# Optimization experiments

Hardware: AMD Instinct MI355X
Metric: run time of the kernel (lower is better)

The kernel has to match this reference:

```python
import jax, jax.numpy as jnp
import numpy as np

T, N = 20, 192
D_EMB, D_H, D_REL = 32, 64, 32
D_TMP = D_REL + 2 * D_H  # 160 = rel_emb + h_self + h_neighbor


def setup_inputs() -> dict:
    key = jax.random.key(0)
    ks = jax.random.split(key, 16)
    g = lambda i, shape, s: jax.random.normal(ks[i], shape, jnp.float32) * s
    inp = {
        "nodes_abs": g(0, (T, N, 2), 1.0),
        "nodes_norm": g(1, (T, N, 2), 1.0),
        "shift_value": g(2, (T, N, 2), 1.0),
        # parameters (inputLayer, LSTMCell, 2 GCNs, outputLayer)
        "w_in": g(3, (D_EMB, 2), 0.2),
        "b_in": jnp.zeros((D_EMB,), jnp.float32),
        "w_ih": g(4, (4 * D_H, D_EMB), 0.1),
        "w_hh": g(5, (4 * D_H, D_H), 0.001),
        "b_ih": jnp.zeros((4 * D_H,), jnp.float32).at[D_H:2 * D_H].set(1.0),
        "b_hh": jnp.zeros((4 * D_H,), jnp.float32),
        "w_rel": g(6, (2, D_REL, 2), 0.1),
        "b_rel": jnp.zeros((2, D_REL), jnp.float32),
        "w_gate": g(7, (2, D_H, D_TMP), 0.1),
        "b_gate": jnp.zeros((2, D_H), jnp.float32),
        "w_ar": g(8, (2, D_TMP), 0.1),
        "b_ar": jnp.zeros((2,), jnp.float32),
        "w_nei": g(9, (2, D_H, D_H), 0.1),
        "w_out": g(10, (2, D_H), 0.1),
        "b_out": jnp.zeros((2,), jnp.float32),
        # int inputs
        "seq_list": jax.random.randint(ks[11], (T, N), 0, 2).astype(jnp.int32),
        "nei_list": jax.random.randint(ks[12], (T, N, N), 0, 2).astype(jnp.int32),
        "nei_num": jax.random.randint(ks[13], (T, N), 0, N).astype(jnp.int32),
    }
    return inp


def reference(nodes_abs, nodes_norm, shift_value, w_in, b_in, w_ih, w_hh, b_ih, b_hh,
              w_rel, b_rel, w_gate, b_gate, w_ar, b_ar, w_nei, w_out, b_out,
              seq_list, nei_list, nei_num):
    eps = 1e-6

    def gcn(p, corr, nei_f, h, c, o):
        # corr: (N,N,2) relative positions pos_i - pos_j; nei_f: (N,N) 0/1 mask
        r = jax.nn.relu(jnp.einsum('ijd,rd->ijr', corr, w_rel[p]) + b_rel[p])
        tmp = jnp.concatenate([r,
                               jnp.broadcast_to(h[:, None, :], (N, N, D_H)),
                               jnp.broadcast_to(h[None, :, :], (N, N, D_H))], axis=-1)
        gate = jax.nn.sigmoid(jnp.einsum('ijt,ht->ijh', tmp, w_gate[p]) + b_gate[p])
        score = jnp.einsum('ijt,t->ij', tmp, w_ar[p]) + b_ar[p]
        score = jnp.where(nei_f > 0, score, -1e9)
        pos = jax.nn.softmax(score, axis=1) * nei_f  # masked attention over neighbors j
        msg = jnp.einsum('ij,ijh,jh->ih', pos, gate, h)  # gated, attended aggregation
        c_new = c + msg @ w_nei[p].T
        h_new = o * jnp.tanh(c_new)
        v1 = jnp.sum(gate * nei_f[:, :, None]) / (jnp.sum(nei_f) * D_H + eps)
        v2 = jnp.sum(jnp.max(pos, axis=1)) / (jnp.sum(jnp.max(nei_f, axis=1)) + eps)
        v3 = jnp.sum(nei_f) / jnp.float32(N)
        return h_new, c_new, (v1, v2, v3)

    def step(carry, xs):
        h, c, v1s, v2s, v3s = carry
        abs_t, norm_t, seq_t, nei_t = xs
        m = seq_t > 0
        mf = m.astype(jnp.float32)
        nei_f = (nei_t > 0).astype(jnp.float32) * mf[:, None] * mf[None, :]
        corr = abs_t[:, None, :] - abs_t[None, :, :]  # corr_index[i,j] = pos_i - pos_j
        x = jax.nn.relu(norm_t @ w_in.T + b_in)  # dropout is identity in eval
        gates = x @ w_ih.T + b_ih + h @ w_hh.T + b_hh
        i_g, f_g, g_g, o_g = jnp.split(gates, 4, axis=-1)
        i_g = jax.nn.sigmoid(i_g); f_g = jax.nn.sigmoid(f_g); o_g = jax.nn.sigmoid(o_g)
        c1 = f_g * c + i_g * jnp.tanh(g_g)
        h1 = o_g * jnp.tanh(c1)
        h1, c1, look = gcn(0, corr, nei_f, h1, c1, o_g)
        h1, c1, _ = gcn(1, corr, nei_f, h1, c1, o_g)
        out_t = (h1 @ w_out.T + b_out) * mf[:, None]
        h = jnp.where(m[:, None], h1, h)  # only active nodes update state
        c = jnp.where(m[:, None], c1, c)
        return (h, c, v1s + look[0], v2s + look[1], v3s + look[2]), out_t

    h0 = jnp.zeros((N, D_H), jnp.float32)
    c0 = jnp.zeros((N, D_H), jnp.float32)
    z = jnp.float32(0.0)
    xs = (nodes_abs[:-1], nodes_norm[:-1], seq_list[:-1], nei_list[:-1])
    (h, c, v1, v2, v3), outs = jax.lax.scan(step, (h0, c0, z, z, z), xs)
    outputs = jnp.concatenate([outs, jnp.zeros((1, N, 2), jnp.float32)], axis=0)
    return outputs, h, c, (v1 / T, v2 / T, v3 / T)
```

## Files before the change

### kernel.cpp

```cpp
#include <hip/hip_runtime.h>
#include <hip/hip_bf16.h>

#define T_STEPS 20
#define NSTEP   19
#define NN      192
#define DH      64
#define DE      32

enum : int {
  O_H     = 0,
  O_C     = O_H    + NN*DH,
  O_UH0   = O_C    + NN*DH,
  O_UH1   = O_UH0  + 2*NN*DH,
  O_CW    = O_UH1  + 2*NN*DH,
  O_OG    = O_CW   + NN*DH,
  O_U1    = O_OG   + NN*DH,
  O_S1    = O_U1   + NN*DH,
  O_S20   = O_S1   + NN,
  O_S21   = O_S20  + NN,
  O_ACC   = O_S21  + NN,
  O_WIHT  = O_ACC  + NSTEP*4 + 4,
  O_WHHT  = O_WIHT + 8192,
  O_BIH   = O_WHHT + 16384,
  O_WIN   = O_BIH  + 256,
  O_BIN   = O_WIN  + 64,
  O_WRELF = O_BIN  + 32,
  O_BRELF = O_WRELF+ 128,
  O_WGR   = O_BRELF+ 64,
  O_WGH1T = O_WGR  + 4096,
  O_WGH2T = O_WGH1T+ 8192,
  O_BGATE = O_WGH2T+ 8192,
  O_WARR  = O_BGATE+ 128,
  O_WARH1 = O_WARR + 64,
  O_WARH2 = O_WARH1+ 128,
  O_BAR   = O_WARH2+ 128,
  O_WNEIT = O_BAR  + 4,
  O_WOUT  = O_WNEIT+ 8192,
  O_BOUT  = O_WOUT + 128,
  O_ISF   = O_BOUT + 2,
  O_TOTAL = O_ISF  + 1
};

typedef unsigned long long ull;

__device__ __forceinline__ float bf2f(__hip_bfloat16 v) { return __bfloat162float(v); }
__device__ __forceinline__ float sigm(float x) { return 1.0f / (1.0f + __expf(-x)); }
__device__ __forceinline__ float tanh_fast(float x) {
  float e = __expf(-2.0f * fabsf(x));
  float r = (1.0f - e) / (1.0f + e);
  return copysignf(r, x);
}

__device__ __forceinline__ float ldf(const void* p, int idx, int isf32) {
  if (isf32) return ((const float*)p)[idx];
  return bf2f(((const __hip_bfloat16*)p)[idx]);
}
__device__ __forceinline__ void stf(void* p, int idx, float v, int isf32) {
  if (isf32) ((float*)p)[idx] = v;
  else       ((__hip_bfloat16*)p)[idx] = __float2bfloat16(v);
}

__device__ __forceinline__ int resolve_isf(const float* F, int isf_arg) {
  return (isf_arg >= 0) ? isf_arg : (int)F[O_ISF];
}

__device__ __forceinline__ void lstm_prep_dev(
    float* __restrict__ F, const void* __restrict__ nnorm, int isf32,
    int t, int i, int tid, int wave, int lane, int load_hc,
    float* s_x, float* s_hc, float* s_cc, float* s_gates, float* s_h1)
{
  if (load_hc && wave == 0) { s_hc[lane] = F[O_H + i*DH + lane]; s_cc[lane] = F[O_C + i*DH + lane]; }
  if (wave == 1 && lane < DE) {
    float nx = ldf(nnorm, (t*NN + i)*2 + 0, isf32);
    float ny = ldf(nnorm, (t*NN + i)*2 + 1, isf32);
    s_x[lane] = fmaxf(nx*F[O_WIN + lane*2] + ny*F[O_WIN + lane*2 + 1] + F[O_BIN + lane], 0.f);
  }
  __syncthreads();
  {
    int G = tid;
    float acc = F[O_BIH + G];
    for (int e = 0; e < DE; e++) acc += F[O_WIHT + e*256 + G] * s_x[e];
    for (int k = 0; k < DH; k++) acc += F[O_WHHT + k*256 + G] * s_hc[k];
    s_gates[G] = acc;
  }
  __syncthreads();
  if (wave == 0) {
    float ig = sigm(s_gates[lane]);
    float fg = sigm(s_gates[64 + lane]);
    float gg = tanh_fast(s_gates[128 + lane]);
    float og = sigm(s_gates[192 + lane]);
    float c1 = fg * s_cc[lane] + ig * gg;
    float h1 = og * tanh_fast(c1);
    int idx = i*DH + lane;
    F[O_CW  + idx] = c1;
    F[O_UH0 + 2*idx + 1] = h1;
    F[O_OG  + idx] = og;
    s_h1[lane] = h1;
  }
  __syncthreads();
  {
    int idx = i*DH + lane;
    if (wave == 0) {
      float a = 0.f;
      const float* w = F + O_WGH1T + lane;
      for (int k = 0; k < DH; k++) a += w[k*DH] * s_h1[k];
      F[O_U1 + idx] = a;
    } else if (wave == 1) {
      float a = 0.f;
      const float* w = F + O_WGH2T + lane;
      for (int k = 0; k < DH; k++) a += w[k*DH] * s_h1[k];
      F[O_UH0 + 2*idx] = a;
    } else if (wave == 2) {
      float hp = s_h1[lane];
      float a1 = hp * F[O_WARH1 + lane];
      float a2 = hp * F[O_WARH2 + lane];
      for (int o = 32; o >= 1; o >>= 1) { a1 += __shfl_xor(a1, o, 64); a2 += __shfl_xor(a2, o, 64); }
      if (lane == 0) { F[O_S1 + i] = a1; F[O_S20 + i] = a2; }
    }
  }
}

__global__ __launch_bounds__(256) void k_init(float* __restrict__ F,
                       void* __restrict__ out,
                       const void* w_in,  const void* b_in,
                       const void* w_ih,  const void* w_hh,
                       const void* b_ih,  const void* b_hh,
                       const void* w_rel, const void* b_rel,
                       const void* w_gate,const void* b_gate,
                       const void* w_ar,  const void* b_ar,
                       const void* w_nei, const void* w_out,
                       const void* b_out, int isf_arg) {
  __shared__ int s_isf;
  const int wave = threadIdx.x >> 6, lane = threadIdx.x & 63;
  if (isf_arg >= 0) {
    if (threadIdx.x == 0) s_isf = isf_arg;
  } else if (wave == 0) {
    const unsigned short* u = (const unsigned short*)w_gate;
    int bad = 0;
    for (int x = lane; x < 1024; x += 64) {
      float v = __uint_as_float(((unsigned)u[x]) << 16);
      if (!(fabsf(v) <= 4.0f)) bad++;
    }
    for (int o = 32; o >= 1; o >>= 1) bad += __shfl_xor(bad, o, 64);
    if (lane == 0) s_isf = (bad > 64);
  }
  __syncthreads();
  const int isf32 = s_isf;
  if (blockIdx.x == 0 && threadIdx.x == 0) F[O_ISF] = (float)isf32;

  int tid = blockIdx.x * blockDim.x + threadIdx.x;
  int stride = gridDim.x * blockDim.x;
  for (int x = tid; x < O_WIHT; x += stride) F[x] = 0.f;
  for (int x = tid; x < NN*2;  x += stride) stf(out, (T_STEPS-1)*NN*2 + x, 0.f, isf32);
  for (int x = tid; x < 8192;  x += stride) { int e = x >> 8, G = x & 255; F[O_WIHT + x] = ldf(w_ih, G*32 + e, isf32); }
  for (int x = tid; x < 16384; x += stride) { int k = x >> 8, G = x & 255; F[O_WHHT + x] = ldf(w_hh, G*64 + k, isf32); }
  for (int x = tid; x < 256;   x += stride) F[O_BIH + x] = ldf(b_ih, x, isf32) + ldf(b_hh, x, isf32);
  for (int x = tid; x < 64;    x += stride) F[O_WIN + x] = ldf(w_in, x, isf32);
  for (int x = tid; x < 32;    x += stride) F[O_BIN + x] = ldf(b_in, x, isf32);
  for (int x = tid; x < 128;   x += stride) F[O_WRELF + x] = ldf(w_rel, x, isf32);
  for (int x = tid; x < 64;    x += stride) F[O_BRELF + x] = ldf(b_rel, x, isf32);
  for (int x = tid; x < 4096;  x += stride) { int p = x >> 11, h = (x >> 5) & 63, d = x & 31;
    F[O_WGR + x] = ldf(w_gate, p*10240 + h*160 + d, isf32); }
  for (int x = tid; x < 8192;  x += stride) { int p = x >> 12, k = (x >> 6) & 63, h = x & 63;
    F[O_WGH1T + x] = ldf(w_gate, p*10240 + h*160 + 32 + k, isf32); }
  for (int x = tid; x < 8192;  x += stride) { int p = x >> 12, k = (x >> 6) & 63, h = x & 63;
    F[O_WGH2T + x] = ldf(w_gate, p*10240 + h*160 + 96 + k, isf32); }
  for (int x = tid; x < 128;   x += stride) F[O_BGATE + x] = ldf(b_gate, x, isf32);
  for (int x = tid; x < 64;    x += stride) { int p = x >> 5, d = x & 31; F[O_WARR + x] = ldf(w_ar, p*160 + d, isf32); }
  for (int x = tid; x < 128;   x += stride) { int p = x >> 6, k = x & 63; F[O_WARH1 + x] = ldf(w_ar, p*160 + 32 + k, isf32); }
  for (int x = tid; x < 128;   x += stride) { int p = x >> 6, k = x & 63; F[O_WARH2 + x] = ldf(w_ar, p*160 + 96 + k, isf32); }
  for (int x = tid; x < 2;     x += stride) F[O_BAR + x] = ldf(b_ar, x, isf32);
  for (int x = tid; x < 8192;  x += stride) { int p = x >> 12, k = (x >> 6) & 63, h = x & 63;
    F[O_WNEIT + x] = ldf(w_nei, p*4096 + h*64 + k, isf32); }
  for (int x = tid; x < 128;   x += stride) F[O_WOUT + x] = ldf(w_out, x, isf32);
  for (int x = tid; x < 2;     x += stride) F[O_BOUT + x] = ldf(b_out, x, isf32);
}

__global__ __launch_bounds__(256) void k_lstm0(float* __restrict__ F,
                                               const void* __restrict__ nnorm,
                                               int isf_arg) {
  __shared__ float s_x[DE], s_hc[DH], s_cc[DH], s_gates[4*DH], s_h1[DH];
  const int tid = threadIdx.x, wave = tid >> 6, lane = tid & 63;
  const int isf32 = resolve_isf(F, isf_arg);
  lstm_prep_dev(F, nnorm, isf32, 0, blockIdx.x, tid, wave, lane, 1,
                s_x, s_hc, s_cc, s_gates, s_h1);
}

__global__ __launch_bounds__(256) void k_gcn(float* __restrict__ F,
                                             const void* __restrict__ nabs,
                                             const void* __restrict__ nnorm,
                                             const int* __restrict__ seq,
                                             const int* __restrict__ nei,
                                             void* __restrict__ out,
                                             int t, int p, int last,
                                             int isf_arg) {
  __shared__ float s_rt[NN*33];
  __shared__ float s_score[NN], s_pos[NN], s_neif[NN];
  __shared__ int   s_jlist[NN];
  __shared__ ull   s_cmask[3];
  __shared__ float s_red[4*DH], s_v1[4], s_msg[DH], s_hprep[DH];
  __shared__ float s_x[DE], s_hc[DH], s_cc[DH], s_gates[4*DH], s_h1[DH];

  const int tid = threadIdx.x, wave = tid >> 6, lane = tid & 63;
  const int i = blockIdx.x;
  const int isf32 = resolve_isf(F, isf_arg);
  const int m_i = seq[t*NN + i] > 0;
  const int UHr = p ? O_UH1 : O_UH0;
  const int S2r = p ? O_S21 : O_S20;

  const int j = wave*64 + lane;
  ull mymask = 0; int nf = 0;
  if (wave < 3) {
    nf = m_i && (seq[t*NN + j] > 0) && (nei[(t*NN + i)*NN + j] > 0);
    s_neif[j] = nf ? 1.f : 0.f;
    mymask = __ballot(nf != 0);
    if (lane == 0) s_cmask[wave] = mymask;
  }
  __syncthreads();
  const int c0 = __popcll(s_cmask[0]), c1 = __popcll(s_cmask[1]), c2 = __popcll(s_cmask[2]);
  const int nv = c0 + c1 + c2;
  if (wave < 3 && nf) {
    int base = (wave == 0) ? 0 : (wave == 1 ? c0 : c0 + c1);
    ull lt = (1ull << lane) - 1ull;
    s_jlist[base + __popcll(mymask & lt)] = j;
  }
  __syncthreads();

  const float2* UH2 = (const float2*)(F + UHr);
  int jc[8]; float2 uc[8];
#pragma unroll
  for (int q = 0; q < 8; q++) {
    int kk = wave + q*4;
    jc[q] = (kk < nv) ? s_jlist[kk] : -1;
    uc[q] = make_float2(0.f, 0.f);
    if (jc[q] >= 0) uc[q] = UH2[jc[q]*DH + lane];
  }
  if (wave < 3) {
    float sc = 0.f;
    if (nf) {
      float cx = ldf(nabs, (t*NN + i)*2 + 0, isf32) - ldf(nabs, (t*NN + j)*2 + 0, isf32);
      float cy = ldf(nabs, (t*NN + i)*2 + 1, isf32) - ldf(nabs, (t*NN + j)*2 + 1, isf32);
      const float* wr = F + O_WRELF + p*64;
      const float* br = F + O_BRELF + p*32;
      const float* wa = F + O_WARR  + p*32;
      float dot = 0.f;
#pragma unroll
      for (int d = 0; d < 32; d++) {
        float rv = fmaxf(cx*wr[2*d] + cy*wr[2*d+1] + br[d], 0.f);
        s_rt[j*33 + d] = rv;
        dot += rv * wa[d];
      }
      sc = dot + F[O_S1 + i] + F[S2r + j] + F[O_BAR + p];
    }
    s_score[j] = sc;
  }
  __syncthreads();

  if (wave == 0) {
    float n0 = s_neif[lane], n1 = s_neif[64+lane], n2 = s_neif[128+lane];
    float sc0 = s_score[lane], sc1 = s_score[64+lane], sc2 = s_score[128+lane];
    const float NEG = -3.0e38f;
    float mx = fmaxf(fmaxf(n0 > 0.f ? sc0 : NEG, n1 > 0.f ? sc1 : NEG),
                     n2 > 0.f ? sc2 : NEG);
    for (int o = 32; o >= 1; o >>= 1) mx = fmaxf(mx, __shfl_xor(mx, o, 64));
    float e0 = (n0 > 0.f) ? __expf(sc0 - mx) : 0.f;
    float e1 = (n1 > 0.f) ? __expf(sc1 - mx) : 0.f;
    float e2 = (n2 > 0.f) ? __expf(sc2 - mx) : 0.f;
    float s = e0 + e1 + e2;
    for (int o = 32; o >= 1; o >>= 1) s += __shfl_xor(s, o, 64);
    float inv = (s > 0.f) ? 1.0f / s : 0.f;
    float p0 = e0*inv, p1 = e1*inv, p2 = e2*inv;
    s_pos[lane] = p0; s_pos[64+lane] = p1; s_pos[128+lane] = p2;
    if (p == 0 && m_i) {
      float cnt = n0 + n1 + n2;
      float pm  = fmaxf(fmaxf(p0, p1), p2);
      for (int o = 32; o >= 1; o >>= 1) {
        cnt += __shfl_xor(cnt, o, 64);
        pm   = fmaxf(pm, __shfl_xor(pm, o, 64));
      }
      if (lane == 0 && cnt > 0.f) {
        atomicAdd(&F[O_ACC + t*4 + 1], cnt);
        atomicAdd(&F[O_ACC + t*4 + 2], pm);
        atomicAdd(&F[O_ACC + t*4 + 3], 1.f);
      }
    }
  }
  __syncthreads();

  {
    float msg = 0.f, v1 = 0.f;
    if (m_i && nv > 0) {
      float wreg[32];
      const float* wgp = F + O_WGR + p*2048 + lane*32;
#pragma unroll
      for (int d = 0; d < 32; d++) wreg[d] = wgp[d];
      float basev = F[O_U1 + i*DH + lane] + F[O_BGATE + p*DH + lane];
      for (int k = wave; k < nv; k += 32) {
        int jn[8]; float2 un[8];
#pragma unroll
        for (int q = 0; q < 8; q++) {
          int kk = k + 32 + q*4;
          jn[q] = (kk < nv) ? s_jlist[kk] : -1;
          un[q] = make_float2(0.f, 0.f);
          if (jn[q] >= 0) un[q] = UH2[jn[q]*DH + lane];
        }
#pragma unroll
        for (int q = 0; q < 8; q++) {
          if (jc[q] >= 0) {
            float acc = basev + uc[q].x;
            const float* rr = &s_rt[jc[q]*33];
#pragma unroll
            for (int d = 0; d < 32; d++) acc += rr[d] * wreg[d];
            float g = sigm(acc);
            v1 += g;
            msg += s_pos[jc[q]] * g * uc[q].y;
          }
        }
#pragma unroll
        for (int q = 0; q < 8; q++) { jc[q] = jn[q]; uc[q] = un[q]; }
      }
    }
    s_red[wave*DH + lane] = msg;
    for (int o = 32; o >= 1; o >>= 1) v1 += __shfl_xor(v1, o, 64);
    if (lane == 0) s_v1[wave] = v1;
  }
  __syncthreads();

  if (wave == 0) {
    s_msg[lane] = s_red[lane] + s_red[64+lane] + s_red[128+lane] + s_red[192+lane];
    if (p == 0 && m_i && lane == 0) {
      float v1t = s_v1[0] + s_v1[1] + s_v1[2] + s_v1[3];
      atomicAdd(&F[O_ACC + t*4 + 0], v1t);
    }
  }
  __syncthreads();

  if (wave == 0) {
    int idx = i*DH + lane;
    float hcom, ccom = 0.f;
    if (m_i) {
      float cn = F[O_CW + idx];
      const float* wn = F + O_WNEIT + p*4096 + lane;
      for (int k = 0; k < DH; k++) cn += s_msg[k] * wn[k*DH];
      hcom = F[O_OG + idx] * tanh_fast(cn);
      F[O_CW + idx] = cn;
      ccom = cn;
      if (p == 1) { F[O_H + idx] = hcom; F[O_C + idx] = ccom; }
    } else {
      hcom = F[UHr + 2*idx + 1];
    }
    if (p == 0) F[O_UH1 + 2*idx + 1] = hcom;
    s_hprep[lane] = hcom;
    if (p == 1) {
      s_hc[lane] = m_i ? hcom : F[O_H + idx];
      s_cc[lane] = m_i ? ccom : F[O_C + idx];
    }
  }
  __syncthreads();

  if (p == 0) {
    int idx = i*DH + lane;
    if (wave == 0) {
      float a = 0.f;
      const float* w = F + O_WGH1T + 4096 + lane;
      for (int k = 0; k < DH; k++) a += w[k*DH] * s_hprep[k];
      F[O_U1 + idx] = a;
    } else if (wave == 1) {
      float a = 0.f;
      const float* w = F + O_WGH2T + 4096 + lane;
      for (int k = 0; k < DH; k++) a += w[k*DH] * s_hprep[k];
      F[O_UH1 + 2*idx] = a;
    } else if (wave == 2) {
      float hp = s_hprep[lane];
      float a1 = hp * F[O_WARH1 + DH + lane];
      float a2 = hp * F[O_WARH2 + DH + lane];
      for (int o = 32; o >= 1; o >>= 1) { a1 += __shfl_xor(a1, o, 64); a2 += __shfl_xor(a2, o, 64); }
      if (lane == 0) { F[O_S1 + i] = a1; F[O_S21 + i] = a2; }
    }
  } else {
    if (wave == 0 && lane < 2) {
      float a = 0.f;
      if (m_i) {
        a = F[O_BOUT + lane];
        const float* wo = F + O_WOUT + lane*DH;
        for (int h = 0; h < DH; h++) a += s_hprep[h] * wo[h];
      }
      stf(out, (t*NN + i)*2 + lane, a, isf32);
    }
    if (!last) {
      lstm_prep_dev(F, nnorm, isf32, t + 1, i, tid, wave, lane, 0,
                    s_x, s_hc, s_cc, s_gates, s_h1);
    } else {
      if (wave == 0) stf(out, T_STEPS*NN*2 + i*DH + lane,         s_hc[lane], isf32);
      if (wave == 1) stf(out, T_STEPS*NN*2 + NN*DH + i*DH + lane, s_cc[lane], isf32);
      if (i == 0 && tid == 0) {
        float v1 = 0.f, v2 = 0.f, v3 = 0.f;
        for (int tt = 0; tt < NSTEP; tt++) {
          float sg = F[O_ACC + tt*4 + 0], sn = F[O_ACC + tt*4 + 1];
          float sp = F[O_ACC + tt*4 + 2], sm = F[O_ACC + tt*4 + 3];
          v1 += sg / (sn * 64.f + 1e-6f);
          v2 += sp / (sm + 1e-6f);
          v3 += sn / 192.f;
        }
        int base = T_STEPS*NN*2 + 2*NN*DH;
        stf(out, base + 0, v1 / 20.f, isf32);
        stf(out, base + 1, v2 / 20.f, isf32);
        stf(out, base + 2, v3 / 20.f, isf32);
      }
    }
  }
}

extern "C" void kernel_launch(void* const* d_in, const int* in_sizes, int n_in,
                              void* d_out, int out_size, void* d_ws, size_t ws_size,
                              hipStream_t stream) {
  const void* nabs  = d_in[0];
  const void* nnorm = d_in[1];
  const int* seq = (const int*)d_in[18];
  const int* nei = (const int*)d_in[19];
  float* F = (float*)d_ws;

  int isf = -1;
  if (n_in > 11 && in_sizes) {
    if      (in_sizes[11] == 81920) isf = 1;
    else if (in_sizes[11] == 40960) isf = 0;
  }

  k_init<<<NN, 256, 0, stream>>>(F, d_out,
      d_in[3], d_in[4], d_in[5], d_in[6], d_in[7], d_in[8], d_in[9], d_in[10],
      d_in[11], d_in[12], d_in[13], d_in[14], d_in[15], d_in[16], d_in[17], isf);
  k_lstm0<<<NN, 256, 0, stream>>>(F, nnorm, isf);
  for (int t = 0; t < NSTEP; t++) {
    k_gcn<<<NN, 256, 0, stream>>>(F, nabs, nnorm, seq, nei, d_out, t, 0, 0, isf);
    k_gcn<<<NN, 256, 0, stream>>>(F, nabs, nnorm, seq, nei, d_out, t, 1, t == NSTEP - 1, isf);
  }
}
```

Before: 697.8 us.

## Fuse all timesteps into one persistent kernel with a software grid barrier

Replaces the 39 per-step kernel launches with a single persistent kernel of 192 blocks that synchronises through an atomic grid barrier using coherent (sc0 sc1) loads and stores. Per-node state (c, og, u1, s1) is kept in shared memory, LSTM weights are held in registers, and the gate and other small weights are cached in LDS, removing repeated global reloads. The rel-gate weight layout is transposed to suit the new LDS access pattern. The risk is deadlock if not all 192 blocks are co-resident, and the spin barrier itself adds latency on every step.

```diff
diff --git a/kernel.cpp b/kernel.cpp
--- a/kernel.cpp
+++ b/kernel.cpp
@@ -19,7 +19,8 @@
   O_S20   = O_S1   + NN,
   O_S21   = O_S20  + NN,
   O_ACC   = O_S21  + NN,
-  O_WIHT  = O_ACC  + NSTEP*4 + 4,
+  O_GBAR  = O_ACC  + NSTEP*4,
+  O_WIHT  = O_GBAR + 4,
   O_WHHT  = O_WIHT + 8192,
   O_BIH   = O_WHHT + 16384,
   O_WIN   = O_BIH  + 256,
@@ -60,64 +61,52 @@
   else       ((__hip_bfloat16*)p)[idx] = __float2bfloat16(v);
 }
 
-__device__ __forceinline__ int resolve_isf(const float* F, int isf_arg) {
-  return (isf_arg >= 0) ? isf_arg : (int)F[O_ISF];
-}
-
-__device__ __forceinline__ void lstm_prep_dev(
-    float* __restrict__ F, const void* __restrict__ nnorm, int isf32,
-    int t, int i, int tid, int wave, int lane, int load_hc,
-    float* s_x, float* s_hc, float* s_cc, float* s_gates, float* s_h1)
-{
-  if (load_hc && wave == 0) { s_hc[lane] = F[O_H + i*DH + lane]; s_cc[lane] = F[O_C + i*DH + lane]; }
-  if (wave == 1 && lane < DE) {
-    float nx = ldf(nnorm, (t*NN + i)*2 + 0, isf32);
-    float ny = ldf(nnorm, (t*NN + i)*2 + 1, isf32);
-    s_x[lane] = fmaxf(nx*F[O_WIN + lane*2] + ny*F[O_WIN + lane*2 + 1] + F[O_BIN + lane], 0.f);
-  }
-  __syncthreads();
-  {
-    int G = tid;
-    float acc = F[O_BIH + G];
-    for (int e = 0; e < DE; e++) acc += F[O_WIHT + e*256 + G] * s_x[e];
-    for (int k = 0; k < DH; k++) acc += F[O_WHHT + k*256 + G] * s_hc[k];
-    s_gates[G] = acc;
-  }
-  __syncthreads();
-  if (wave == 0) {
-    float ig = sigm(s_gates[lane]);
-    float fg = sigm(s_gates[64 + lane]);
-    float gg = tanh_fast(s_gates[128 + lane]);
-    float og = sigm(s_gates[192 + lane]);
-    float c1 = fg * s_cc[lane] + ig * gg;
-    float h1 = og * tanh_fast(c1);
-    int idx = i*DH + lane;
-    F[O_CW  + idx] = c1;
-    F[O_UH0 + 2*idx + 1] = h1;
-    F[O_OG  + idx] = og;
-    s_h1[lane] = h1;
-  }
-  __syncthreads();
-  {
-    int idx = i*DH + lane;
-    if (wave == 0) {
-      float a = 0.f;
-      const float* w = F + O_WGH1T + lane;
-      for (int k = 0; k < DH; k++) a += w[k*DH] * s_h1[k];
-      F[O_U1 + idx] = a;
-    } else if (wave == 1) {
-      float a = 0.f;
-      const float* w = F + O_WGH2T + lane;
-      for (int k = 0; k < DH; k++) a += w[k*DH] * s_h1[k];
-      F[O_UH0 + 2*idx] = a;
-    } else if (wave == 2) {
-      float hp = s_h1[lane];
-      float a1 = hp * F[O_WARH1 + lane];
-      float a2 = hp * F[O_WARH2 + lane];
-      for (int o = 32; o >= 1; o >>= 1) { a1 += __shfl_xor(a1, o, 64); a2 += __shfl_xor(a2, o, 64); }
-      if (lane == 0) { F[O_S1 + i] = a1; F[O_S20 + i] = a2; }
+__device__ __forceinline__ ull ld_coh_u64_async(const void* p) {
+  ull v;
+  asm volatile("global_load_dwordx2 %0, %1, off sc0 sc1" : "=v"(v) : "v"(p));
+  return v;
+}
+__device__ __forceinline__ float ld_coh_f32_async(const void* p) {
+  float v;
+  asm volatile("global_load_dword %0, %1, off sc0 sc1" : "=v"(v) : "v"(p));
+  return v;
+}
+__device__ __forceinline__ float ld_coh_f32(const void* p) {
+  float v;
+  asm volatile("global_load_dword %0, %1, off sc0 sc1\n\ts_waitcnt vmcnt(0)"
+               : "=v"(v) : "v"(p) : "memory");
+  return v;
+}
+__device__ __forceinline__ unsigned ld_coh_u32(const void* p) {
+  unsigned v;
+  asm volatile("global_load_dword %0, %1, off sc0 sc1\n\ts_waitcnt vmcnt(0)"
+               : "=v"(v) : "v"(p) : "memory");
+  return v;
+}
+__device__ __forceinline__ void st_coh_f32(void* p, float v) {
+  asm volatile("global_store_dword %0, %1, off sc0 sc1" :: "v"(p), "v"(v) : "memory");
+}
+__device__ __forceinline__ void st_coh_u32(void* p, unsigned v) {
+  asm volatile("global_store_dword %0, %1, off sc0 sc1" :: "v"(p), "v"(v) : "memory");
+}
+__device__ __forceinline__ void vm_wait0() {
+  asm volatile("s_waitcnt vmcnt(0)" ::: "memory");
+  __builtin_amdgcn_sched_barrier(0);
+}
+
+__device__ __forceinline__ void gridbar(float* F, unsigned ep) {
+  asm volatile("s_waitcnt vmcnt(0)" ::: "memory");
+  __syncthreads();
+  if (threadIdx.x == 0) {
+    unsigned* bar = (unsigned*)(F + O_GBAR);
+    unsigned v = atomicAdd(bar, 1u) + 1u;
+    if (v == (ep + 1u) * (unsigned)NN) {
+      st_coh_u32(bar + 1, ep + 1u);
+    } else {
+      while (ld_coh_u32(bar + 1) < ep + 1u) __builtin_amdgcn_s_sleep(2);
     }
   }
+  __syncthreads();
 }
 
 __global__ __launch_bounds__(256) void k_init(float* __restrict__ F,
@@ -159,7 +148,7 @@
   for (int x = tid; x < 32;    x += stride) F[O_BIN + x] = ldf(b_in, x, isf32);
   for (int x = tid; x < 128;   x += stride) F[O_WRELF + x] = ldf(w_rel, x, isf32);
   for (int x = tid; x < 64;    x += stride) F[O_BRELF + x] = ldf(b_rel, x, isf32);
-  for (int x = tid; x < 4096;  x += stride) { int p = x >> 11, h = (x >> 5) & 63, d = x & 31;
+  for (int x = tid; x < 4096;  x += stride) { int p = x >> 11, d = (x >> 6) & 31, h = x & 63;
     F[O_WGR + x] = ldf(w_gate, p*10240 + h*160 + d, isf32); }
   for (int x = tid; x < 8192;  x += stride) { int p = x >> 12, k = (x >> 6) & 63, h = x & 63;
     F[O_WGH1T + x] = ldf(w_gate, p*10240 + h*160 + 32 + k, isf32); }
@@ -176,236 +165,302 @@
   for (int x = tid; x < 2;     x += stride) F[O_BOUT + x] = ldf(b_out, x, isf32);
 }
 
-__global__ __launch_bounds__(256) void k_lstm0(float* __restrict__ F,
-                                               const void* __restrict__ nnorm,
-                                               int isf_arg) {
-  __shared__ float s_x[DE], s_hc[DH], s_cc[DH], s_gates[4*DH], s_h1[DH];
-  const int tid = threadIdx.x, wave = tid >> 6, lane = tid & 63;
-  const int isf32 = resolve_isf(F, isf_arg);
-  lstm_prep_dev(F, nnorm, isf32, 0, blockIdx.x, tid, wave, lane, 1,
-                s_x, s_hc, s_cc, s_gates, s_h1);
-}
-
-__global__ __launch_bounds__(256) void k_gcn(float* __restrict__ F,
-                                             const void* __restrict__ nabs,
-                                             const void* __restrict__ nnorm,
-                                             const int* __restrict__ seq,
-                                             const int* __restrict__ nei,
-                                             void* __restrict__ out,
-                                             int t, int p, int last,
-                                             int isf_arg) {
+__device__ __forceinline__ void lstm_prep(
+    float* __restrict__ F, const void* __restrict__ nnorm, int isf32,
+    int t, int i, int tid, int wave, int lane,
+    const float* wih_r, const float* whh_r, float bih_r,
+    const float* s_win, const float* s_cB,
+    float* s_x, float* s_hc, float* s_cc, float* s_gates, float* s_h1,
+    float* s_cw, float* s_og, float* s_u1, float* s_s1)
+{
+  if (wave == 1 && lane < DE) {
+    float nx = ldf(nnorm, (t*NN + i)*2 + 0, isf32);
+    float ny = ldf(nnorm, (t*NN + i)*2 + 1, isf32);
+    s_x[lane] = fmaxf(nx*s_win[lane*2] + ny*s_win[lane*2 + 1] + s_win[64 + lane], 0.f);
+  }
+  __syncthreads();
+  {
+    float acc = bih_r;
+#pragma unroll
+    for (int e = 0; e < DE; e++) acc += wih_r[e] * s_x[e];
+#pragma unroll
+    for (int k = 0; k < DH; k++) acc += whh_r[k] * s_hc[k];
+    s_gates[tid] = acc;
+  }
+  __syncthreads();
+  if (wave == 0) {
+    float ig = sigm(s_gates[lane]);
+    float fg = sigm(s_gates[64 + lane]);
+    float gg = tanh_fast(s_gates[128 + lane]);
+    float og = sigm(s_gates[192 + lane]);
+    float c1 = fg * s_cc[lane] + ig * gg;
+    float h1 = og * tanh_fast(c1);
+    s_cw[lane] = c1;
+    s_og[lane] = og;
+    s_h1[lane] = h1;
+    st_coh_f32(F + O_UH0 + 2*(i*DH + lane) + 1, h1);
+  }
+  __syncthreads();
+  if (wave == 0) {
+    float a = 0.f;
+    const float* w = F + O_WGH1T + lane;
+    for (int k = 0; k < DH; k++) a += w[k*DH] * s_h1[k];
+    s_u1[lane] = a;
+  } else if (wave == 1) {
+    float a = 0.f;
+    const float* w = F + O_WGH2T + lane;
+    for (int k = 0; k < DH; k++) a += w[k*DH] * s_h1[k];
+    st_coh_f32(F + O_UH0 + 2*(i*DH + lane), a);
+  } else if (wave == 2) {
+    float hp = s_h1[lane];
+    float a1 = hp * s_cB[192 + lane];
+    float a2 = hp * s_cB[320 + lane];
+    for (int o = 32; o >= 1; o >>= 1) { a1 += __shfl_xor(a1, o, 64); a2 += __shfl_xor(a2, o, 64); }
+    if (lane == 0) { *s_s1 = a1; st_coh_f32(F + O_S20 + i, a2); }
+  }
+}
+
+__global__ __launch_bounds__(256, 1) void k_main(float* __restrict__ F,
+    const void* __restrict__ nabs, const void* __restrict__ nnorm,
+    const int* __restrict__ seq, const int* __restrict__ nei,
+    void* __restrict__ out, int isf_arg)
+{
   __shared__ float s_rt[NN*33];
   __shared__ float s_score[NN], s_pos[NN], s_neif[NN];
   __shared__ int   s_jlist[NN];
   __shared__ ull   s_cmask[3];
   __shared__ float s_red[4*DH], s_v1[4], s_msg[DH], s_hprep[DH];
   __shared__ float s_x[DE], s_hc[DH], s_cc[DH], s_gates[4*DH], s_h1[DH];
+  __shared__ float s_cw[DH], s_og[DH], s_u1[DH], s_s1;
+  __shared__ float s_wgt[4096];
+  __shared__ float s_cA[192], s_cB[452], s_cC[130], s_win[96];
+  __shared__ float s_fin[NSTEP*4];
 
   const int tid = threadIdx.x, wave = tid >> 6, lane = tid & 63;
   const int i = blockIdx.x;
-  const int isf32 = resolve_isf(F, isf_arg);
-  const int m_i = seq[t*NN + i] > 0;
-  const int UHr = p ? O_UH1 : O_UH0;
-  const int S2r = p ? O_S21 : O_S20;
-
-  const int j = wave*64 + lane;
-  ull mymask = 0; int nf = 0;
-  if (wave < 3) {
-    nf = m_i && (seq[t*NN + j] > 0) && (nei[(t*NN + i)*NN + j] > 0);
-    s_neif[j] = nf ? 1.f : 0.f;
-    mymask = __ballot(nf != 0);
-    if (lane == 0) s_cmask[wave] = mymask;
-  }
-  __syncthreads();
-  const int c0 = __popcll(s_cmask[0]), c1 = __popcll(s_cmask[1]), c2 = __popcll(s_cmask[2]);
-  const int nv = c0 + c1 + c2;
-  if (wave < 3 && nf) {
-    int base = (wave == 0) ? 0 : (wave == 1 ? c0 : c0 + c1);
-    ull lt = (1ull << lane) - 1ull;
-    s_jlist[base + __popcll(mymask & lt)] = j;
-  }
-  __syncthreads();
-
-  const float2* UH2 = (const float2*)(F + UHr);
-  int jc[8]; float2 uc[8];
-#pragma unroll
-  for (int q = 0; q < 8; q++) {
-    int kk = wave + q*4;
-    jc[q] = (kk < nv) ? s_jlist[kk] : -1;
-    uc[q] = make_float2(0.f, 0.f);
-    if (jc[q] >= 0) uc[q] = UH2[jc[q]*DH + lane];
-  }
-  if (wave < 3) {
-    float sc = 0.f;
-    if (nf) {
-      float cx = ldf(nabs, (t*NN + i)*2 + 0, isf32) - ldf(nabs, (t*NN + j)*2 + 0, isf32);
-      float cy = ldf(nabs, (t*NN + i)*2 + 1, isf32) - ldf(nabs, (t*NN + j)*2 + 1, isf32);
-      const float* wr = F + O_WRELF + p*64;
-      const float* br = F + O_BRELF + p*32;
-      const float* wa = F + O_WARR  + p*32;
-      float dot = 0.f;
-#pragma unroll
-      for (int d = 0; d < 32; d++) {
-        float rv = fmaxf(cx*wr[2*d] + cy*wr[2*d+1] + br[d], 0.f);
-        s_rt[j*33 + d] = rv;
-        dot += rv * wa[d];
-      }
-      sc = dot + F[O_S1 + i] + F[S2r + j] + F[O_BAR + p];
+  const int isf32 = (isf_arg >= 0) ? isf_arg : (int)F[O_ISF];
+
+  float wih_r[DE], whh_r[DH];
+  const float bih_r = F[O_BIH + tid];
+#pragma unroll
+  for (int e = 0; e < DE; e++) wih_r[e] = F[O_WIHT + e*256 + tid];
+#pragma unroll
+  for (int k = 0; k < DH; k++) whh_r[k] = F[O_WHHT + k*256 + tid];
+
+  for (int x = tid; x < 4096; x += 256) s_wgt[x] = F[O_WGR + x];
+  for (int x = tid; x < 192; x += 256) s_cA[x] = F[O_WRELF + x];
+  for (int x = tid; x < 452; x += 256) s_cB[x] = F[O_BGATE + x];
+  for (int x = tid; x < 130; x += 256) s_cC[x] = F[O_WOUT + x];
+  for (int x = tid; x < 96;  x += 256) s_win[x] = F[O_WIN + x];
+  if (wave == 0) { s_hc[lane] = 0.f; s_cc[lane] = 0.f; }
+  __syncthreads();
+
+  lstm_prep(F, nnorm, isf32, 0, i, tid, wave, lane,
+            wih_r, whh_r, bih_r, s_win, s_cB,
+            s_x, s_hc, s_cc, s_gates, s_h1, s_cw, s_og, s_u1, &s_s1);
+
+  unsigned ep = 0;
+  for (int t = 0; t < NSTEP; ++t) {
+    const int m_i = seq[t*NN + i] > 0;
+    const int j = wave*64 + lane;
+
+    ull mymask = 0; int nf = 0;
+    if (wave < 3) {
+      nf = m_i && (seq[t*NN + j] > 0) && (nei[(t*NN + i)*NN + j] > 0);
+      s_neif[j] = nf ? 1.f : 0.f;
+      mymask = __ballot(nf != 0);
+      if (lane == 0) s_cmask[wave] = mymask;
     }
-    s_score[j] = sc;
-  }
-  __syncthreads();
-
-  if (wave == 0) {
-    float n0 = s_neif[lane], n1 = s_neif[64+lane], n2 = s_neif[128+lane];
-    float sc0 = s_score[lane], sc1 = s_score[64+lane], sc2 = s_score[128+lane];
-    const float NEG = -3.0e38f;
-    float mx = fmaxf(fmaxf(n0 > 0.f ? sc0 : NEG, n1 > 0.f ? sc1 : NEG),
-                     n2 > 0.f ? sc2 : NEG);
-    for (int o = 32; o >= 1; o >>= 1) mx = fmaxf(mx, __shfl_xor(mx, o, 64));
-    float e0 = (n0 > 0.f) ? __expf(sc0 - mx) : 0.f;
-    float e1 = (n1 > 0.f) ? __expf(sc1 - mx) : 0.f;
-    float e2 = (n2 > 0.f) ? __expf(sc2 - mx) : 0.f;
-    float s = e0 + e1 + e2;
-    for (int o = 32; o >= 1; o >>= 1) s += __shfl_xor(s, o, 64);
-    float inv = (s > 0.f) ? 1.0f / s : 0.f;
-    float p0 = e0*inv, p1 = e1*inv, p2 = e2*inv;
-    s_pos[lane] = p0; s_pos[64+lane] = p1; s_pos[128+lane] = p2;
-    if (p == 0 && m_i) {
-      float cnt = n0 + n1 + n2;
-      float pm  = fmaxf(fmaxf(p0, p1), p2);
-      for (int o = 32; o >= 1; o >>= 1) {
-        cnt += __shfl_xor(cnt, o, 64);
-        pm   = fmaxf(pm, __shfl_xor(pm, o, 64));
-      }
-      if (lane == 0 && cnt > 0.f) {
-        atomicAdd(&F[O_ACC + t*4 + 1], cnt);
-        atomicAdd(&F[O_ACC + t*4 + 2], pm);
-        atomicAdd(&F[O_ACC + t*4 + 3], 1.f);
-      }
+    __syncthreads();
+    const int c0 = __popcll(s_cmask[0]), c1 = __popcll(s_cmask[1]);
+    const int nv = c0 + c1 + __popcll(s_cmask[2]);
+    if (wave < 3 && nf) {
+      int base = (wave == 0) ? 0 : ((wave == 1) ? c0 : c0 + c1);
+      ull lt = (1ull << lane) - 1ull;
+      s_jlist[base + __popcll(mymask & lt)] = j;
     }
-  }
-  __syncthreads();
-
-  {
-    float msg = 0.f, v1 = 0.f;
-    if (m_i && nv > 0) {
-      float wreg[32];
-      const float* wgp = F + O_WGR + p*2048 + lane*32;
-#pragma unroll
-      for (int d = 0; d < 32; d++) wreg[d] = wgp[d];
-      float basev = F[O_U1 + i*DH + lane] + F[O_BGATE + p*DH + lane];
-      for (int k = wave; k < nv; k += 32) {
-        int jn[8]; float2 un[8];
-#pragma unroll
-        for (int q = 0; q < 8; q++) {
-          int kk = k + 32 + q*4;
-          jn[q] = (kk < nv) ? s_jlist[kk] : -1;
-          un[q] = make_float2(0.f, 0.f);
-          if (jn[q] >= 0) un[q] = UH2[jn[q]*DH + lane];
-        }
-#pragma unroll
-        for (int q = 0; q < 8; q++) {
-          if (jc[q] >= 0) {
-            float acc = basev + uc[q].x;
-            const float* rr = &s_rt[jc[q]*33];
-#pragma unroll
-            for (int d = 0; d < 32; d++) acc += rr[d] * wreg[d];
-            float g = sigm(acc);
-            v1 += g;
-            msg += s_pos[jc[q]] * g * uc[q].y;
-          }
-        }
-#pragma unroll
-        for (int q = 0; q < 8; q++) { jc[q] = jn[q]; uc[q] = un[q]; }
-      }
-    }
-    s_red[wave*DH + lane] = msg;
-    for (int o = 32; o >= 1; o >>= 1) v1 += __shfl_xor(v1, o, 64);
-    if (lane == 0) s_v1[wave] = v1;
-  }
-  __syncthreads();
-
-  if (wave == 0) {
-    s_msg[lane] = s_red[lane] + s_red[64+lane] + s_red[128+lane] + s_red[192+lane];
-    if (p == 0 && m_i && lane == 0) {
-      float v1t = s_v1[0] + s_v1[1] + s_v1[2] + s_v1[3];
-      atomicAdd(&F[O_ACC + t*4 + 0], v1t);
-    }
-  }
-  __syncthreads();
-
-  if (wave == 0) {
-    int idx = i*DH + lane;
-    float hcom, ccom = 0.f;
-    if (m_i) {
-      float cn = F[O_CW + idx];
-      const float* wn = F + O_WNEIT + p*4096 + lane;
-      for (int k = 0; k < DH; k++) cn += s_msg[k] * wn[k*DH];
-      hcom = F[O_OG + idx] * tanh_fast(cn);
-      F[O_CW + idx] = cn;
-      ccom = cn;
-      if (p == 1) { F[O_H + idx] = hcom; F[O_C + idx] = ccom; }
-    } else {
-      hcom = F[UHr + 2*idx + 1];
-    }
-    if (p == 0) F[O_UH1 + 2*idx + 1] = hcom;
-    s_hprep[lane] = hcom;
-    if (p == 1) {
-      s_hc[lane] = m_i ? hcom : F[O_H + idx];
-      s_cc[lane] = m_i ? ccom : F[O_C + idx];
-    }
-  }
-  __syncthreads();
-
-  if (p == 0) {
-    int idx = i*DH + lane;
-    if (wave == 0) {
-      float a = 0.f;
-      const float* w = F + O_WGH1T + 4096 + lane;
-      for (int k = 0; k < DH; k++) a += w[k*DH] * s_hprep[k];
-      F[O_U1 + idx] = a;
-    } else if (wave == 1) {
-      float a = 0.f;
-      const float* w = F + O_WGH2T + 4096 + lane;
-      for (int k = 0; k < DH; k++) a += w[k*DH] * s_hprep[k];
-      F[O_UH1 + 2*idx] = a;
-    } else if (wave == 2) {
-      float hp = s_hprep[lane];
-      float a1 = hp * F[O_WARH1 + DH + lane];
-      float a2 = hp * F[O_WARH2 + DH + lane];
-      for (int o = 32; o >= 1; o >>= 1) { a1 += __shfl_xor(a1, o, 64); a2 += __shfl_xor(a2, o, 64); }
-      if (lane == 0) { F[O_S1 + i] = a1; F[O_S21 + i] = a2; }
-    }
-  } else {
-    if (wave == 0 && lane < 2) {
-      float a = 0.f;
-      if (m_i) {
-        a = F[O_BOUT + lane];
-        const float* wo = F + O_WOUT + lane*DH;
-        for (int h = 0; h < DH; h++) a += s_hprep[h] * wo[h];
-      }
-      stf(out, (t*NN + i)*2 + lane, a, isf32);
-    }
-    if (!last) {
-      lstm_prep_dev(F, nnorm, isf32, t + 1, i, tid, wave, lane, 0,
-                    s_x, s_hc, s_cc, s_gates, s_h1);
-    } else {
-      if (wave == 0) stf(out, T_STEPS*NN*2 + i*DH + lane,         s_hc[lane], isf32);
-      if (wave == 1) stf(out, T_STEPS*NN*2 + NN*DH + i*DH + lane, s_cc[lane], isf32);
-      if (i == 0 && tid == 0) {
-        float v1 = 0.f, v2 = 0.f, v3 = 0.f;
-        for (int tt = 0; tt < NSTEP; tt++) {
-          float sg = F[O_ACC + tt*4 + 0], sn = F[O_ACC + tt*4 + 1];
-          float sp = F[O_ACC + tt*4 + 2], sm = F[O_ACC + tt*4 + 3];
-          v1 += sg / (sn * 64.f + 1e-6f);
-          v2 += sp / (sm + 1e-6f);
-          v3 += sn / 192.f;
-        }
-        int base = T_STEPS*NN*2 + 2*NN*DH;
-        stf(out, base + 0, v1 / 20.f, isf32);
-        stf(out, base + 1, v2 / 20.f, isf32);
-        stf(out, base + 2, v3 / 20.f, isf32);
+
+    for (int p = 0; p < 2; ++p) {
+      gridbar(F, ep++);
+      const int last = (t == NSTEP - 1) && (p == 1);
+      const int UHr = p ? O_UH1 : O_UH0;
+      const int S2r = p ? O_S21 : O_S20;
+
+      if (wave < 3) {
+        float s2j = ld_coh_f32_async(F + S2r + j);
+        float sc = 0.f, dot = 0.f;
+        if (nf) {
+          float cx = ldf(nabs, (t*NN + i)*2 + 0, isf32) - ldf(nabs, (t*NN + j)*2 + 0, isf32);
+          float cy = ldf(nabs, (t*NN + i)*2 + 1, isf32) - ldf(nabs, (t*NN + j)*2 + 1, isf32);
+          const float* wr = s_cA + p*64;
+          const float* br = s_cA + 128 + p*32;
+          const float* wa = s_cB + 128 + p*32;
+#pragma unroll
+          for (int d = 0; d < 32; d++) {
+            float rv = fmaxf(cx*wr[2*d] + cy*wr[2*d+1] + br[d], 0.f);
+            s_rt[j*33 + d] = rv;
+            dot += rv * wa[d];
+          }
+        }
+        vm_wait0();
+        if (nf) sc = dot + s_s1 + s2j + s_cB[448 + p];
+        s_score[j] = sc;
+      }
+      __syncthreads();
+
+      if (wave == 0) {
+        float n0 = s_neif[lane], n1 = s_neif[64+lane], n2 = s_neif[128+lane];
+        float sc0 = s_score[lane], sc1 = s_score[64+lane], sc2 = s_score[128+lane];
+        const float NEG = -3.0e38f;
+        float mx = fmaxf(fmaxf(n0 > 0.f ? sc0 : NEG, n1 > 0.f ? sc1 : NEG),
+                         n2 > 0.f ? sc2 : NEG);
+        for (int o = 32; o >= 1; o >>= 1) mx = fmaxf(mx, __shfl_xor(mx, o, 64));
+        float e0 = (n0 > 0.f) ? __expf(sc0 - mx) : 0.f;
+        float e1 = (n1 > 0.f) ? __expf(sc1 - mx) : 0.f;
+        float e2 = (n2 > 0.f) ? __expf(sc2 - mx) : 0.f;
+        float s = e0 + e1 + e2;
+        for (int o = 32; o >= 1; o >>= 1) s += __shfl_xor(s, o, 64);
+        float inv = (s > 0.f) ? 1.0f / s : 0.f;
+        float p0 = e0*inv, p1 = e1*inv, p2 = e2*inv;
+        s_pos[lane] = p0; s_pos[64+lane] = p1; s_pos[128+lane] = p2;
+        if (p == 0 && m_i) {
+          float cnt = n0 + n1 + n2;
+          float pm  = fmaxf(fmaxf(p0, p1), p2);
+          for (int o = 32; o >= 1; o >>= 1) {
+            cnt += __shfl_xor(cnt, o, 64);
+            pm   = fmaxf(pm, __shfl_xor(pm, o, 64));
+          }
+          if (lane == 0 && cnt > 0.f) {
+            atomicAdd(&F[O_ACC + t*4 + 1], cnt);
+            atomicAdd(&F[O_ACC + t*4 + 2], pm);
+            atomicAdd(&F[O_ACC + t*4 + 3], 1.f);
+          }
+        }
+      }
+      __syncthreads();
+
+      {
+        float msg = 0.f, v1 = 0.f;
+        if (m_i && nv > 0) {
+          float wreg[32];
+#pragma unroll
+          for (int d = 0; d < 32; d++) wreg[d] = s_wgt[p*2048 + d*64 + lane];
+          float basev = s_u1[lane] + s_cB[p*DH + lane];
+          const float* UHbase = F + UHr;
+          for (int c = 0; c < 6; ++c) {
+            int k0 = wave + c*32;
+            if (k0 >= nv) break;
+            int jv[8]; ull u[8];
+#pragma unroll
+            for (int m = 0; m < 8; m++) {
+              int kk = k0 + 4*m;
+              jv[m] = (kk < nv) ? s_jlist[kk] : 0;
+              u[m] = ld_coh_u64_async(UHbase + 2*(jv[m]*DH + lane));
+            }
+            vm_wait0();
+#pragma unroll
+            for (int m = 0; m < 8; m++) {
+              int kk = k0 + 4*m;
+              if (kk < nv) {
+                float ux = __uint_as_float((unsigned)u[m]);
+                float uy = __uint_as_float((unsigned)(u[m] >> 32));
+                float acc = basev + ux;
+                const float* rr = &s_rt[jv[m]*33];
+#pragma unroll
+                for (int d = 0; d < 32; d++) acc += rr[d] * wreg[d];
+                float g = sigm(acc);
+                v1 += g;
+                msg += s_pos[jv[m]] * g * uy;
+              }
+            }
+          }
+        }
+        s_red[wave*DH + lane] = msg;
+        for (int o = 32; o >= 1; o >>= 1) v1 += __shfl_xor(v1, o, 64);
+        if (lane == 0) s_v1[wave] = v1;
+      }
+      __syncthreads();
+
+      if (wave == 0) {
+        s_msg[lane] = s_red[lane] + s_red[64+lane] + s_red[128+lane] + s_red[192+lane];
+        if (p == 0 && m_i && lane == 0) {
+          atomicAdd(&F[O_ACC + t*4 + 0], s_v1[0] + s_v1[1] + s_v1[2] + s_v1[3]);
+        }
+      }
+      __syncthreads();
+
+      if (wave == 0) {
+        float hcom, ccom = 0.f;
+        if (m_i) {
+          float cn = s_cw[lane];
+          const float* wn = F + O_WNEIT + p*4096 + lane;
+          for (int k = 0; k < DH; k++) cn += s_msg[k] * wn[k*DH];
+          hcom = s_og[lane] * tanh_fast(cn);
+          s_cw[lane] = cn;
+          ccom = cn;
+        } else {
+          hcom = p ? s_hprep[lane] : s_h1[lane];
+        }
+        if (p == 0) st_coh_f32(F + O_UH1 + 2*(i*DH + lane) + 1, hcom);
+        s_hprep[lane] = hcom;
+        if (p == 1 && m_i) { s_hc[lane] = hcom; s_cc[lane] = ccom; }
+      }
+      __syncthreads();
+
+      if (p == 0) {
+        if (wave == 0) {
+          float a = 0.f;
+          const float* w = F + O_WGH1T + 4096 + lane;
+          for (int k = 0; k < DH; k++) a += w[k*DH] * s_hprep[k];
+          s_u1[lane] = a;
+        } else if (wave == 1) {
+          float a = 0.f;
+          const float* w = F + O_WGH2T + 4096 + lane;
+          for (int k = 0; k < DH; k++) a += w[k*DH] * s_hprep[k];
+          st_coh_f32(F + O_UH1 + 2*(i*DH + lane), a);
+        } else if (wave == 2) {
+          float hp = s_hprep[lane];
+          float a1 = hp * s_cB[192 + DH + lane];
+          float a2 = hp * s_cB[320 + DH + lane];
+          for (int o = 32; o >= 1; o >>= 1) { a1 += __shfl_xor(a1, o, 64); a2 += __shfl_xor(a2, o, 64); }
+          if (lane == 0) { s_s1 = a1; st_coh_f32(F + O_S21 + i, a2); }
+        }
+      } else {
+        if (wave == 0 && lane < 2) {
+          float a = 0.f;
+          if (m_i) {
+            a = s_cC[128 + lane];
+            const float* wo = s_cC + lane*DH;
+            for (int h = 0; h < DH; h++) a += s_hprep[h] * wo[h];
+          }
+          stf(out, (t*NN + i)*2 + lane, a, isf32);
+        }
+        if (!last) {
+          lstm_prep(F, nnorm, isf32, t + 1, i, tid, wave, lane,
+                    wih_r, whh_r, bih_r, s_win, s_cB,
+                    s_x, s_hc, s_cc, s_gates, s_h1, s_cw, s_og, s_u1, &s_s1);
+        } else {
+          if (wave == 0) stf(out, T_STEPS*NN*2 + i*DH + lane,         s_hc[lane], isf32);
+          if (wave == 1) stf(out, T_STEPS*NN*2 + NN*DH + i*DH + lane, s_cc[lane], isf32);
+          if (i == 0) {
+            if (tid < NSTEP*4) s_fin[tid] = ld_coh_f32(F + O_ACC + tid);
+            __syncthreads();
+            if (tid == 0) {
+              float v1 = 0.f, v2 = 0.f, v3 = 0.f;
+              for (int tt = 0; tt < NSTEP; tt++) {
+                float sg = s_fin[tt*4 + 0], sn = s_fin[tt*4 + 1];
+                float sp = s_fin[tt*4 + 2], sm = s_fin[tt*4 + 3];
+                v1 += sg / (sn * 64.f + 1e-6f);
+                v2 += sp / (sm + 1e-6f);
+                v3 += sn / 192.f;
+              }
+              int base = T_STEPS*NN*2 + 2*NN*DH;
+              stf(out, base + 0, v1 / 20.f, isf32);
+              stf(out, base + 1, v2 / 20.f, isf32);
+              stf(out, base + 2, v3 / 20.f, isf32);
+            }
+          }
+        }
       }
     }
   }
@@ -429,9 +484,5 @@
   k_init<<<NN, 256, 0, stream>>>(F, d_out,
       d_in[3], d_in[4], d_in[5], d_in[6], d_in[7], d_in[8], d_in[9], d_in[10],
       d_in[11], d_in[12], d_in[13], d_in[14], d_in[15], d_in[16], d_in[17], isf);
-  k_lstm0<<<NN, 256, 0, stream>>>(F, nnorm, isf);
-  for (int t = 0; t < NSTEP; t++) {
-    k_gcn<<<NN, 256, 0, stream>>>(F, nabs, nnorm, seq, nei, d_out, t, 0, 0, isf);
-    k_gcn<<<NN, 256, 0, stream>>>(F, nabs, nnorm, seq, nei, d_out, t, 1, t == NSTEP - 1, isf);
-  }
-}
+  k_main<<<NN, 256, 0, stream>>>(F, nabs, nnorm, seq, nei, d_out, isf);
+}
```

Measured after the change: 1.296 ms. +85.7%, slower.
